# Kernel tuning notes

Hardware: AMD Instinct MI355X
Metric: run time of the kernel (lower is better)

Reference implementation:

```python
import jax, jax.numpy as jnp
import numpy as np

jax.config.update("jax_enable_x64", True)

POOL = np.array([4.0, 4.0, 4.0], dtype=np.float32)  # pool_size
N, E, D, B = 400_000, 3_200_000, 64, 16


def setup_inputs() -> dict:
    key = jax.random.key(0)
    k1, k2, k3, k4 = jax.random.split(key, 4)
    x = jax.random.normal(k1, (N, D), dtype=jnp.float32)
    pos = jax.random.uniform(k2, (N, 3), dtype=jnp.float32) * 128.0
    batch = jnp.sort(jax.random.randint(k3, (N,), 0, B)).astype(jnp.int64)
    edge_index = jax.random.randint(k4, (E, 2), 0, N).astype(jnp.int64)
    return {"x": x, "pos": pos, "edge_index": edge_index, "batch": batch}


def _voxel_key(pos, batch):
    # torch.div(pos, pool, rounding_mode='floor').long()
    qpos = jnp.floor(pos / jnp.asarray(POOL)).astype(jnp.int64)  # [N,3]
    strides = [int(qpos[:, i].max()) + 1 for i in range(3)]
    k = batch.astype(jnp.int64)
    for i in range(3):
        k = k * strides[i] + qpos[:, i]  # linearized (batch, qx, qy, qz) key
    return k, strides


def reference(x, pos, edge_index, batch):
    keyv, s = _voxel_key(pos, batch)
    ukey, inv = jnp.unique(keyv, return_inverse=True)  # unique voxel keys
    M = int(ukey.shape[0])
    new_batch = ukey // (s[0] * s[1] * s[2])  # recover batch id from key prefix

    # average_positions=True: scatter-mean of pos (include_self=False == pure mean)
    counts = jax.ops.segment_sum(jnp.ones((pos.shape[0],), pos.dtype), inv, num_segments=M)
    pos_mean = jax.ops.segment_sum(pos, inv, num_segments=M) / counts[:, None]

    # scatter-reduce amax of features (every segment non-empty by construction)
    pooled_x = jax.ops.segment_max(x, inv, num_segments=M)

    # remap edges, drop self-loops, dedup, append self-loops for all M nodes
    ei = inv[edge_index]  # [E,2]
    mask = ei[:, 0] != ei[:, 1]
    enc = ei[:, 0].astype(jnp.int64) * M + ei[:, 1].astype(jnp.int64)
    uenc = jnp.unique(enc[mask])
    ei_dedup = jnp.stack([uenc // M, uenc % M], axis=1)
    ar = jnp.arange(M, dtype=ei_dedup.dtype)
    loops = jnp.stack([ar, ar], axis=1)
    ei_out = jnp.concatenate([ei_dedup, loops], axis=0)

    return pooled_x, pos_mean, ei_out, new_batch
```

## Files before the change

kernel.cpp:

```cpp
#include <hip/hip_runtime.h>


#define KSP 524288
#define SCAN_BLOCK 256
#define SCAN_ITEMS 16
#define SCAN_CHUNK 4096
#define NCHUNK (KSP / SCAN_CHUNK)
#define NPART 1024
#define PB 512
#define SCAP2 8192


__global__ void k_qmax(const float* __restrict__ pos, unsigned* hdr, int N) {
  __shared__ unsigned sm[3];
  if (threadIdx.x < 3) sm[threadIdx.x] = 0;
  __syncthreads();
  int i = blockIdx.x * blockDim.x + threadIdx.x;
  if (i < N) {
    int q0 = (int)floorf(pos[3 * i + 0] * 0.25f);
    int q1 = (int)floorf(pos[3 * i + 1] * 0.25f);
    int q2 = (int)floorf(pos[3 * i + 2] * 0.25f);
    atomicMax(&sm[0], (unsigned)q0);
    atomicMax(&sm[1], (unsigned)q1);
    atomicMax(&sm[2], (unsigned)q2);
  }
  __syncthreads();
  if (threadIdx.x < 3) atomicMax(&hdr[threadIdx.x], sm[threadIdx.x]);
}

__global__ void k_keys(const float* __restrict__ pos, const int* __restrict__ batch,
                       const unsigned* __restrict__ hdr, unsigned* __restrict__ key,
                       unsigned* __restrict__ cnt, int N) {
  int i = blockIdx.x * blockDim.x + threadIdx.x;
  if (i >= N) return;
  unsigned s0 = hdr[0] + 1, s1 = hdr[1] + 1, s2 = hdr[2] + 1;
  unsigned q0 = (unsigned)(int)floorf(pos[3 * i + 0] * 0.25f);
  unsigned q1 = (unsigned)(int)floorf(pos[3 * i + 1] * 0.25f);
  unsigned q2 = (unsigned)(int)floorf(pos[3 * i + 2] * 0.25f);
  unsigned k = (((unsigned)batch[i] * s0 + q0) * s1 + q1) * s2 + q2;
  key[i] = k;
  atomicAdd(&cnt[k], 1u);
}

__global__ void scanA(const unsigned* __restrict__ in, unsigned* __restrict__ out,
                      unsigned* __restrict__ chunkSums, int n, int presence) {
  __shared__ unsigned lds[SCAN_BLOCK];
  int tbase = blockIdx.x * SCAN_CHUNK + threadIdx.x * SCAN_ITEMS;
  unsigned vals[SCAN_ITEMS];
  unsigned sum = 0;
  for (int i = 0; i < SCAN_ITEMS; ++i) {
    unsigned v = 0;
    int idx = tbase + i;
    if (idx < n) { v = in[idx]; if (presence) v = v ? 1u : 0u; }
    vals[i] = sum;
    sum += v;
  }
  lds[threadIdx.x] = sum;
  __syncthreads();
  for (int off = 1; off < SCAN_BLOCK; off <<= 1) {
    unsigned t = (threadIdx.x >= (unsigned)off) ? lds[threadIdx.x - off] : 0u;
    __syncthreads();
    lds[threadIdx.x] += t;
    __syncthreads();
  }
  unsigned threadExcl = lds[threadIdx.x] - sum;
  for (int i = 0; i < SCAN_ITEMS; ++i) {
    int idx = tbase + i;
    if (idx < n) out[idx] = threadExcl + vals[i];
  }
  if (threadIdx.x == SCAN_BLOCK - 1) chunkSums[blockIdx.x] = lds[SCAN_BLOCK - 1];
}

__global__ void scanB(unsigned* chunkSums, unsigned* totalDst, int nchunks) {
  __shared__ unsigned lds[1024];
  unsigned v = (threadIdx.x < (unsigned)nchunks) ? chunkSums[threadIdx.x] : 0u;
  lds[threadIdx.x] = v;
  __syncthreads();
  for (int off = 1; off < 1024; off <<= 1) {
    unsigned t = (threadIdx.x >= (unsigned)off) ? lds[threadIdx.x - off] : 0u;
    __syncthreads();
    lds[threadIdx.x] += t;
    __syncthreads();
  }
  if (threadIdx.x < (unsigned)nchunks) chunkSums[threadIdx.x] = lds[threadIdx.x] - v;
  if (threadIdx.x == 0 && totalDst) *totalDst = lds[1023];
}

__global__ void scanC(unsigned* __restrict__ out, unsigned* __restrict__ out2,
                      const unsigned* __restrict__ chunkSums, int n) {
  int idx = blockIdx.x * blockDim.x + threadIdx.x;
  if (idx >= n) return;
  unsigned v = out[idx] + chunkSums[idx / SCAN_CHUNK];
  out[idx] = v;
  if (out2) out2[idx] = v;
}

__global__ void k_scan1024(const unsigned* __restrict__ in, unsigned* __restrict__ outStart,
                           unsigned* __restrict__ outCursor, unsigned* __restrict__ totalDst) {
  __shared__ unsigned lds[NPART];
  unsigned t = threadIdx.x;
  unsigned v = in[t];
  lds[t] = v;
  __syncthreads();
  for (int off = 1; off < NPART; off <<= 1) {
    unsigned x = (t >= (unsigned)off) ? lds[t - off] : 0u;
    __syncthreads();
    lds[t] += x;
    __syncthreads();
  }
  unsigned excl = lds[t] - v;
  outStart[t] = excl;
  if (outCursor) outCursor[t] = excl;
  if (t == NPART - 1) {
    outStart[NPART] = lds[t];
    if (totalDst) *totalDst = lds[t];
  }
}

__global__ void k_ukey(const unsigned* __restrict__ cnt, const unsigned* __restrict__ rank,
                       unsigned* __restrict__ ukeyArr) {
  int k = blockIdx.x * blockDim.x + threadIdx.x;
  if (k >= KSP) return;
  if (cnt[k]) ukeyArr[rank[k]] = (unsigned)k;
}

__global__ void k_scatter(const unsigned* __restrict__ key, const unsigned* __restrict__ rank,
                          unsigned* __restrict__ inv, unsigned* __restrict__ ptCursor,
                          unsigned* __restrict__ ptOrder, int N) {
  int i = blockIdx.x * blockDim.x + threadIdx.x;
  if (i >= N) return;
  unsigned k = key[i];
  inv[i] = rank[k];
  unsigned posn = atomicAdd(&ptCursor[k], 1u);
  ptOrder[posn] = (unsigned)i;
}

__global__ void k_cstart(const unsigned* __restrict__ cnt, const unsigned* __restrict__ rank,
                         const unsigned* __restrict__ ptStart, const unsigned* __restrict__ hdr,
                         unsigned* __restrict__ cStart, int N) {
  int k = blockIdx.x * blockDim.x + threadIdx.x;
  if (k >= KSP) return;
  if (cnt[k]) cStart[rank[k]] = ptStart[k];
  if (k == 0) cStart[hdr[3]] = (unsigned)N;
}

__global__ void __launch_bounds__(256) k_pool(const float4* __restrict__ x4,
                                              const float* __restrict__ pos,
                                              const unsigned* __restrict__ ptOrder,
                                              const unsigned* __restrict__ cStart,
                                              const unsigned* __restrict__ hdr,
                                              float* __restrict__ out) {
  unsigned gtid = blockIdx.x * blockDim.x + threadIdx.x;
  unsigned m = gtid >> 3;
  unsigned l = gtid & 7u;
  unsigned M = hdr[3];
  if (m >= M) return;
  unsigned start = cStart[m];
  unsigned n = cStart[m + 1] - start;
  const float NI = -__builtin_huge_valf();
  float4 a0 = make_float4(NI, NI, NI, NI);
  float4 a1 = a0;
  float psum = 0.0f;
  for (unsigned j = 0; j < n; ++j) {
    unsigned p = ptOrder[start + j];
    float4 v0 = x4[p * 16u + l];
    float4 v1 = x4[p * 16u + 8u + l];
    a0.x = fmaxf(a0.x, v0.x); a0.y = fmaxf(a0.y, v0.y);
    a0.z = fmaxf(a0.z, v0.z); a0.w = fmaxf(a0.w, v0.w);
    a1.x = fmaxf(a1.x, v1.x); a1.y = fmaxf(a1.y, v1.y);
    a1.z = fmaxf(a1.z, v1.z); a1.w = fmaxf(a1.w, v1.w);
    if (l < 3) psum += pos[3u * p + l];
  }
  float4* o4 = (float4*)out;
  o4[m * 16u + l] = a0;
  o4[m * 16u + 8u + l] = a1;
  if (l < 3) {
    unsigned long long O1 = 64ull * M;
    out[O1 + 3ull * m + l] = psum / (float)n;
  }
}

__global__ void __launch_bounds__(256) k_ehist2(const int2* __restrict__ ei,
                                                const unsigned* __restrict__ inv,
                                                unsigned* __restrict__ partCnt, int E, int span) {
  __shared__ unsigned h[NPART];
  for (int i = threadIdx.x; i < NPART; i += 256) h[i] = 0;
  __syncthreads();
  int lo = blockIdx.x * span;
  int hi = min(E, lo + span);
  for (int e = lo + threadIdx.x; e < hi; e += 256) {
    int2 pr = ei[e];
    unsigned a = inv[pr.x], b = inv[pr.y];
    if (a != b) atomicAdd(&h[a >> 9], 1u);
  }
  __syncthreads();
  for (int i = threadIdx.x; i < NPART; i += 256) {
    unsigned v = h[i];
    if (v) atomicAdd(&partCnt[i], v);
  }
}

__global__ void __launch_bounds__(256) k_pscatter(const int2* __restrict__ ei,
                                                  const unsigned* __restrict__ inv,
                                                  unsigned* __restrict__ partCursor,
                                                  unsigned long long* __restrict__ pStage,
                                                  int E, int span) {
  __shared__ unsigned h[NPART];
  for (int i = threadIdx.x; i < NPART; i += 256) h[i] = 0;
  __syncthreads();
  int lo = blockIdx.x * span;
  int hi = min(E, lo + span);
  for (int e = lo + threadIdx.x; e < hi; e += 256) {
    int2 pr = ei[e];
    unsigned a = inv[pr.x], b = inv[pr.y];
    if (a != b) atomicAdd(&h[a >> 9], 1u);
  }
  __syncthreads();
  for (int i = threadIdx.x; i < NPART; i += 256) {
    unsigned v = h[i];
    h[i] = v ? atomicAdd(&partCursor[i], v) : 0u;
  }
  __syncthreads();
  for (int e = lo + threadIdx.x; e < hi; e += 256) {
    int2 pr = ei[e];
    unsigned a = inv[pr.x], b = inv[pr.y];
    if (a != b) {
      unsigned off = atomicAdd(&h[a >> 9], 1u);
      pStage[off] = ((unsigned long long)a << 19) | b;
    }
  }
}

__global__ void __launch_bounds__(256) k_bucket(unsigned long long* __restrict__ pStage,
                                                const unsigned* __restrict__ partStart,
                                                unsigned* __restrict__ partDistinct) {
  __shared__ unsigned dstL[SCAP2];
  __shared__ unsigned h[PB];
  __shared__ unsigned bbase[PB + 1];
  __shared__ unsigned stmp[256];
  unsigned p = blockIdx.x;
  unsigned s = partStart[p];
  unsigned c = partStart[p + 1] - s;
  unsigned t = threadIdx.x;
  for (int i = t; i < PB; i += 256) h[i] = 0;
  __syncthreads();
  if (c <= SCAP2) {
    const unsigned* lo32 = (const unsigned*)(pStage + s);
    for (unsigned i = t; i < c; i += 256) {
      unsigned code28 = lo32[2 * i] & 0x0FFFFFFFu;
      atomicAdd(&h[code28 >> 19], 1u);
    }
    __syncthreads();
    {
      unsigned a = h[2 * t], b = h[2 * t + 1], sum = a + b;
      stmp[t] = sum;
      __syncthreads();
      for (int off = 1; off < 256; off <<= 1) {
        unsigned x = (t >= (unsigned)off) ? stmp[t - off] : 0u;
        __syncthreads(); stmp[t] += x; __syncthreads();
      }
      unsigned excl = stmp[t] - sum;
      bbase[2 * t] = excl; bbase[2 * t + 1] = excl + a;
      if (t == 255) bbase[PB] = stmp[255];
    }
    __syncthreads();
    for (int i = t; i < PB; i += 256) h[i] = bbase[i];
    __syncthreads();
    for (unsigned i = t; i < c; i += 256) {
      unsigned code28 = lo32[2 * i] & 0x0FFFFFFFu;
      unsigned off = atomicAdd(&h[code28 >> 19], 1u);
      dstL[off] = code28;
    }
    __syncthreads();
    unsigned L = (c + 255) >> 8;
    unsigned vv[32], rr[32];
#pragma unroll
    for (unsigned k = 0; k < 32; ++k) {
      unsigned i = t * L + k;
      if (k < L && i < c) {
        unsigned v = dstL[i];
        unsigned b = v >> 19;
        unsigned blo = bbase[b], bhi = bbase[b + 1];
        unsigned r = blo;
        for (unsigned j = blo; j < bhi; ++j) {
          unsigned u = dstL[j];
          r += (u < v) || (u == v && j < i);
        }
        vv[k] = v; rr[k] = r;
      }
    }
    __syncthreads();
#pragma unroll
    for (unsigned k = 0; k < 32; ++k) {
      unsigned i = t * L + k;
      if (k < L && i < c) dstL[rr[k]] = vv[k];
    }
    __syncthreads();
    unsigned flm = 0, localSum = 0;
#pragma unroll
    for (unsigned k = 0; k < 32; ++k) {
      unsigned i = t * L + k;
      if (k < L && i < c) {
        unsigned v = dstL[i];
        unsigned pv = dstL[i - (i > 0 ? 1u : 0u)];
        unsigned f = (i == 0) | (pv != v);
        flm |= f << k;
        localSum += f;
      }
    }
    stmp[t] = localSum;
    __syncthreads();
    for (int off = 1; off < 256; off <<= 1) {
      unsigned x = (t >= (unsigned)off) ? stmp[t - off] : 0u;
      __syncthreads(); stmp[t] += x; __syncthreads();
    }
    unsigned pos = stmp[t] - localSum;
    unsigned long long pbase = (unsigned long long)p << 28;
#pragma unroll
    for (unsigned k = 0; k < 32; ++k) {
      unsigned i = t * L + k;
      if (k < L && i < c && ((flm >> k) & 1u)) {
        pStage[s + pos] = pbase | (unsigned long long)dstL[i];
        ++pos;
      }
    }
    if (t == 255) partDistinct[p] = stmp[255];
  } else if (t == 0) {
    for (unsigned i = 1; i < c; ++i) {
      unsigned long long v = pStage[s + i];
      long long j = (long long)i - 1;
      while (j >= 0 && pStage[s + j] > v) { pStage[s + j + 1] = pStage[s + j]; --j; }
      pStage[s + j + 1] = v;
    }
    unsigned d = 0;
    unsigned long long prev = ~0ull;
    for (unsigned i = 0; i < c; ++i) {
      unsigned long long v = pStage[s + i];
      if (i == 0 || v != prev) { pStage[s + d] = v; ++d; }
      prev = v;
    }
    partDistinct[p] = d;
  }
}

__global__ void __launch_bounds__(256) k_ewriteP(const unsigned long long* __restrict__ pStage,
                                                 const unsigned* __restrict__ partStart,
                                                 const unsigned* __restrict__ partOut,
                                                 const unsigned* __restrict__ hdr,
                                                 float* __restrict__ out) {
  unsigned p = blockIdx.x;
  unsigned s = partStart[p];
  unsigned rbase = partOut[p];
  unsigned d = partOut[p + 1] - rbase;
  unsigned M = hdr[3];
  unsigned long long O2 = 67ull * M;
  for (unsigned j = threadIdx.x; j < d; j += 256) {
    unsigned long long code = pStage[s + j];
    unsigned long long row = (unsigned long long)rbase + j;
    out[O2 + 2 * row + 0] = (float)(unsigned)(code >> 19);
    out[O2 + 2 * row + 1] = (float)(unsigned)(code & 0x7FFFFu);
  }
}

__global__ void k_final(const unsigned* __restrict__ ukeyArr, const unsigned* __restrict__ hdr,
                        float* __restrict__ out) {
  unsigned m = blockIdx.x * blockDim.x + threadIdx.x;
  unsigned M = hdr[3];
  if (m >= M) return;
  unsigned Ed = hdr[5];
  unsigned long long O2 = 67ull * M;
  unsigned long long row = (unsigned long long)Ed + m;
  float fm = (float)m;
  out[O2 + 2 * row + 0] = fm;
  out[O2 + 2 * row + 1] = fm;
  unsigned s0 = hdr[0] + 1, s1 = hdr[1] + 1, s2 = hdr[2] + 1;
  unsigned vol = s0 * s1 * s2;
  unsigned long long O3 = O2 + 2ull * (Ed + M);
  out[O3 + m] = (float)(ukeyArr[m] / vol);
}

extern "C" void kernel_launch(void* const* d_in, const int* in_sizes, int n_in,
                              void* d_out, int out_size, void* d_ws, size_t ws_size,
                              hipStream_t stream) {
  const float* x = (const float*)d_in[0];
  const float* pos = (const float*)d_in[1];
  const int* ei = (const int*)d_in[2];
  const int* batch = (const int*)d_in[3];
  float* out = (float*)d_out;
  int N = in_sizes[3];
  int E = in_sizes[2] / 2;

  unsigned* ws = (unsigned*)d_ws;
  unsigned* hdr          = ws;
  unsigned* cnt          = ws + 64;
  unsigned* partCnt      = cnt + KSP;
  unsigned* partDistinct = partCnt + NPART;
  unsigned* rank         = partDistinct + NPART;
  unsigned* ukeyArr      = rank + KSP;
  unsigned* partStart    = ukeyArr + KSP;
  unsigned* partCursor   = partStart + NPART + 2;
  unsigned* partOut      = partCursor + NPART;
  unsigned* chunkSums    = partOut + NPART + 2;
  unsigned* key          = chunkSums + 1024;
  unsigned* inv          = key + N;
  unsigned* pS32         = inv + ((N + 1) & ~1);
  unsigned long long* pStage = (unsigned long long*)pS32;
  unsigned* ptStart  = pS32;
  unsigned* ptCursor = pS32 + KSP;
  unsigned* ptOrder  = pS32 + 2 * KSP;
  unsigned* cStart   = ptCursor;

  hipMemsetAsync(ws, 0, (size_t)(64 + KSP + 2 * NPART) * 4, stream);

  const int B = 256;
  int gN = (N + B - 1) / B;
  int gK = (KSP + B - 1) / B;
  int gP = (int)(((long long)N * 8 + B - 1) / B);
  int span = (E + 255) / 256;

  k_qmax<<<gN, B, 0, stream>>>(pos, hdr, N);
  k_keys<<<gN, B, 0, stream>>>(pos, batch, hdr, key, cnt, N);

  scanA<<<NCHUNK, SCAN_BLOCK, 0, stream>>>(cnt, rank, chunkSums, KSP, 1);
  scanB<<<1, 1024, 0, stream>>>(chunkSums, &hdr[3], NCHUNK);
  scanC<<<gK, B, 0, stream>>>(rank, nullptr, chunkSums, KSP);

  scanA<<<NCHUNK, SCAN_BLOCK, 0, stream>>>(cnt, ptStart, chunkSums, KSP, 0);
  scanB<<<1, 1024, 0, stream>>>(chunkSums, &hdr[6], NCHUNK);
  scanC<<<gK, B, 0, stream>>>(ptStart, ptCursor, chunkSums, KSP);

  k_ukey<<<gK, B, 0, stream>>>(cnt, rank, ukeyArr);
  k_scatter<<<gN, B, 0, stream>>>(key, rank, inv, ptCursor, ptOrder, N);
  k_cstart<<<gK, B, 0, stream>>>(cnt, rank, ptStart, hdr, cStart, N);
  k_pool<<<gP, B, 0, stream>>>((const float4*)x, pos, ptOrder, cStart, hdr, out);

  const int2* ei2 = (const int2*)ei;
  k_ehist2<<<256, 256, 0, stream>>>(ei2, inv, partCnt, E, span);
  k_scan1024<<<1, NPART, 0, stream>>>(partCnt, partStart, partCursor, &hdr[4]);
  k_pscatter<<<256, 256, 0, stream>>>(ei2, inv, partCursor, pStage, E, span);
  k_bucket<<<NPART, 256, 0, stream>>>(pStage, partStart, partDistinct);
  k_scan1024<<<1, NPART, 0, stream>>>(partDistinct, partOut, nullptr, &hdr[5]);
  k_ewriteP<<<NPART, 256, 0, stream>>>(pStage, partStart, partOut, hdr, out);
  k_final<<<gK, B, 0, stream>>>(ukeyArr, hdr, out);

  (void)n_in; (void)ws_size;
}
```

Measured before the change: 525.5 us.

## Compact edge staging to 32-bit codes and register-cache edges in scatter

Edge codes in the staging buffer shrink from 64-bit to 32-bit by dropping the partition prefix, which is rebuilt from the block index when the output is written. The scatter kernel keeps each thread's 16 edge codes in registers between the count and write phases, so edges and their inv entries are no longer re-read. Both edge kernels also launch far more blocks (2048 for the histogram, about 782 for the scatter) instead of 256. The aim is less memory traffic and more parallelism in the edge dedup pipeline, at the cost of higher register pressure in the scatter kernel.

```diff
diff --git a/kernel.cpp b/kernel.cpp
--- a/kernel.cpp
+++ b/kernel.cpp
@@ -9,6 +9,7 @@
 #define NPART 1024
 #define PB 512
 #define SCAP2 8192
+#define PS_ITERS 16
 
 
 __global__ void k_qmax(const float* __restrict__ pos, unsigned* hdr, int N) {
@@ -203,17 +204,25 @@
 __global__ void __launch_bounds__(256) k_pscatter(const int2* __restrict__ ei,
                                                   const unsigned* __restrict__ inv,
                                                   unsigned* __restrict__ partCursor,
-                                                  unsigned long long* __restrict__ pStage,
-                                                  int E, int span) {
+                                                  unsigned* __restrict__ pStage,
+                                                  int E) {
   __shared__ unsigned h[NPART];
   for (int i = threadIdx.x; i < NPART; i += 256) h[i] = 0;
   __syncthreads();
-  int lo = blockIdx.x * span;
-  int hi = min(E, lo + span);
-  for (int e = lo + threadIdx.x; e < hi; e += 256) {
-    int2 pr = ei[e];
-    unsigned a = inv[pr.x], b = inv[pr.y];
-    if (a != b) atomicAdd(&h[a >> 9], 1u);
+  int lo = blockIdx.x * (256 * PS_ITERS);
+  unsigned long long codes[PS_ITERS];
+#pragma unroll
+  for (int it = 0; it < PS_ITERS; ++it) {
+    codes[it] = ~0ull;
+    int e = lo + threadIdx.x + it * 256;
+    if (e < E) {
+      int2 pr = ei[e];
+      unsigned a = inv[pr.x], b = inv[pr.y];
+      if (a != b) {
+        codes[it] = ((unsigned long long)a << 19) | b;
+        atomicAdd(&h[a >> 9], 1u);
+      }
+    }
   }
   __syncthreads();
   for (int i = threadIdx.x; i < NPART; i += 256) {
@@ -221,17 +230,18 @@
     h[i] = v ? atomicAdd(&partCursor[i], v) : 0u;
   }
   __syncthreads();
-  for (int e = lo + threadIdx.x; e < hi; e += 256) {
-    int2 pr = ei[e];
-    unsigned a = inv[pr.x], b = inv[pr.y];
-    if (a != b) {
+#pragma unroll
+  for (int it = 0; it < PS_ITERS; ++it) {
+    unsigned long long code = codes[it];
+    if (code != ~0ull) {
+      unsigned a = (unsigned)(code >> 19);
       unsigned off = atomicAdd(&h[a >> 9], 1u);
-      pStage[off] = ((unsigned long long)a << 19) | b;
-    }
-  }
-}
-
-__global__ void __launch_bounds__(256) k_bucket(unsigned long long* __restrict__ pStage,
+      pStage[off] = ((a & 511u) << 19) | ((unsigned)code & 0x7FFFFu);
+    }
+  }
+}
+
+__global__ void __launch_bounds__(256) k_bucket(unsigned* __restrict__ pStage,
                                                 const unsigned* __restrict__ partStart,
                                                 unsigned* __restrict__ partDistinct) {
   __shared__ unsigned dstL[SCAP2];
@@ -245,10 +255,9 @@
   for (int i = t; i < PB; i += 256) h[i] = 0;
   __syncthreads();
   if (c <= SCAP2) {
-    const unsigned* lo32 = (const unsigned*)(pStage + s);
+    const unsigned* src = pStage + s;
     for (unsigned i = t; i < c; i += 256) {
-      unsigned code28 = lo32[2 * i] & 0x0FFFFFFFu;
-      atomicAdd(&h[code28 >> 19], 1u);
+      atomicAdd(&h[src[i] >> 19], 1u);
     }
     __syncthreads();
     {
@@ -267,7 +276,7 @@
     for (int i = t; i < PB; i += 256) h[i] = bbase[i];
     __syncthreads();
     for (unsigned i = t; i < c; i += 256) {
-      unsigned code28 = lo32[2 * i] & 0x0FFFFFFFu;
+      unsigned code28 = src[i];
       unsigned off = atomicAdd(&h[code28 >> 19], 1u);
       dstL[off] = code28;
     }
@@ -315,35 +324,34 @@
       __syncthreads(); stmp[t] += x; __syncthreads();
     }
     unsigned pos = stmp[t] - localSum;
-    unsigned long long pbase = (unsigned long long)p << 28;
 #pragma unroll
     for (unsigned k = 0; k < 32; ++k) {
       unsigned i = t * L + k;
       if (k < L && i < c && ((flm >> k) & 1u)) {
-        pStage[s + pos] = pbase | (unsigned long long)dstL[i];
+        pStage[s + pos] = dstL[i];
         ++pos;
       }
     }
     if (t == 255) partDistinct[p] = stmp[255];
   } else if (t == 0) {
+    unsigned* a = pStage + s;
     for (unsigned i = 1; i < c; ++i) {
-      unsigned long long v = pStage[s + i];
+      unsigned v = a[i];
       long long j = (long long)i - 1;
-      while (j >= 0 && pStage[s + j] > v) { pStage[s + j + 1] = pStage[s + j]; --j; }
-      pStage[s + j + 1] = v;
-    }
-    unsigned d = 0;
-    unsigned long long prev = ~0ull;
+      while (j >= 0 && a[j] > v) { a[j + 1] = a[j]; --j; }
+      a[j + 1] = v;
+    }
+    unsigned d = 0, prev = 0xFFFFFFFFu;
     for (unsigned i = 0; i < c; ++i) {
-      unsigned long long v = pStage[s + i];
-      if (i == 0 || v != prev) { pStage[s + d] = v; ++d; }
+      unsigned v = a[i];
+      if (i == 0 || v != prev) { a[d] = v; ++d; }
       prev = v;
     }
     partDistinct[p] = d;
   }
 }
 
-__global__ void __launch_bounds__(256) k_ewriteP(const unsigned long long* __restrict__ pStage,
+__global__ void __launch_bounds__(256) k_ewriteP(const unsigned* __restrict__ pStage,
                                                  const unsigned* __restrict__ partStart,
                                                  const unsigned* __restrict__ partOut,
                                                  const unsigned* __restrict__ hdr,
@@ -354,11 +362,12 @@
   unsigned d = partOut[p + 1] - rbase;
   unsigned M = hdr[3];
   unsigned long long O2 = 67ull * M;
+  unsigned pbase = p << 9;
   for (unsigned j = threadIdx.x; j < d; j += 256) {
-    unsigned long long code = pStage[s + j];
+    unsigned code = pStage[s + j];
     unsigned long long row = (unsigned long long)rbase + j;
-    out[O2 + 2 * row + 0] = (float)(unsigned)(code >> 19);
-    out[O2 + 2 * row + 1] = (float)(unsigned)(code & 0x7FFFFu);
+    out[O2 + 2 * row + 0] = (float)(pbase | (code >> 19));
+    out[O2 + 2 * row + 1] = (float)(code & 0x7FFFFu);
   }
 }
 
@@ -404,7 +413,7 @@
   unsigned* key          = chunkSums + 1024;
   unsigned* inv          = key + N;
   unsigned* pS32         = inv + ((N + 1) & ~1);
-  unsigned long long* pStage = (unsigned long long*)pS32;
+  unsigned* pStage       = pS32;
   unsigned* ptStart  = pS32;
   unsigned* ptCursor = pS32 + KSP;
   unsigned* ptOrder  = pS32 + 2 * KSP;
@@ -416,7 +425,9 @@
   int gN = (N + B - 1) / B;
   int gK = (KSP + B - 1) / B;
   int gP = (int)(((long long)N * 8 + B - 1) / B);
-  int span = (E + 255) / 256;
+  int ebH = 2048;
+  int spanH = (E + ebH - 1) / ebH;
+  int ebS = (E + 256 * PS_ITERS - 1) / (256 * PS_ITERS);
 
   k_qmax<<<gN, B, 0, stream>>>(pos, hdr, N);
   k_keys<<<gN, B, 0, stream>>>(pos, batch, hdr, key, cnt, N);
@@ -435,9 +446,9 @@
   k_pool<<<gP, B, 0, stream>>>((const float4*)x, pos, ptOrder, cStart, hdr, out);
 
   const int2* ei2 = (const int2*)ei;
-  k_ehist2<<<256, 256, 0, stream>>>(ei2, inv, partCnt, E, span);
+  k_ehist2<<<ebH, 256, 0, stream>>>(ei2, inv, partCnt, E, spanH);
   k_scan1024<<<1, NPART, 0, stream>>>(partCnt, partStart, partCursor, &hdr[4]);
-  k_pscatter<<<256, 256, 0, stream>>>(ei2, inv, partCursor, pStage, E, span);
+  k_pscatter<<<ebS, 256, 0, stream>>>(ei2, inv, partCursor, pStage, E);
   k_bucket<<<NPART, 256, 0, stream>>>(pStage, partStart, partDistinct);
   k_scan1024<<<1, NPART, 0, stream>>>(partDistinct, partOut, nullptr, &hdr[5]);
   k_ewriteP<<<NPART, 256, 0, stream>>>(pStage, partStart, partOut, hdr, out);
```

Measured after the change: 520.8 us. About the same (-0.9%).
